# Kernel optimization log

Measured on AMD Instinct MI355X. Metric: run time of the kernel, lower is better.

## Reference

```python
import jax, jax.numpy as jnp
import numpy as np

B, S, HID = 2, 2048, 2048
NH, NKV, HD = 32, 8, 64
EPS = 1e-6
SCALE = HD ** -0.5


def rms_norm(x, w, eps=EPS):
    xf = x.astype(jnp.float32)
    var = jnp.mean(xf * xf, axis=-1, keepdims=True)
    return (w * (xf * jax.lax.rsqrt(var + eps))).astype(x.dtype)


def rotate_half(x):
    x1, x2 = jnp.split(x, 2, axis=-1)
    return jnp.concatenate((-x2, x1), axis=-1)


def setup_inputs() -> dict:
    key = jax.random.key(0)
    ks = jax.random.split(key, 8)
    hidden_states = jax.random.normal(ks[0], (B, S, HID), jnp.float32)
    # realistic RoPE tables
    inv_freq = 1.0 / (500000.0 ** (np.arange(0, HD, 2, dtype=np.float32) / HD))
    pos = np.arange(S, dtype=np.float32)
    freqs = np.outer(pos, inv_freq)                      # [S, HD/2]
    emb = np.concatenate([freqs, freqs], axis=-1)        # [S, HD]
    cos = jnp.broadcast_to(jnp.asarray(np.cos(emb)), (B, S, HD))
    sin = jnp.broadcast_to(jnp.asarray(np.sin(emb)), (B, S, HD))
    std = HID ** -0.5
    Wq = jax.random.normal(ks[1], (NH * HD, HID), jnp.float32) * std
    Wk = jax.random.normal(ks[2], (NKV * HD, HID), jnp.float32) * std
    Wv = jax.random.normal(ks[3], (NKV * HD, HID), jnp.float32) * std
    Wo = jax.random.normal(ks[4], (HID, NH * HD), jnp.float32) * std
    q_norm_w = jnp.ones((HD,), jnp.float32)
    k_norm_w = jnp.ones((HD,), jnp.float32)
    return {"hidden_states": hidden_states, "cos": cos, "sin": sin,
            "Wq": Wq, "Wk": Wk, "Wv": Wv, "Wo": Wo,
            "q_norm_w": q_norm_w, "k_norm_w": k_norm_w}


def reference(hidden_states, cos, sin, Wq, Wk, Wv, Wo, q_norm_w, k_norm_w):
    b, s, _ = hidden_states.shape
    # QKV projections (nn.Linear: x @ W.T)
    q = (hidden_states @ Wq.T).reshape(b, s, NH, HD).transpose(0, 2, 1, 3)   # [B,NH,S,D]
    k = (hidden_states @ Wk.T).reshape(b, s, NKV, HD).transpose(0, 2, 1, 3)  # [B,NKV,S,D]
    v = (hidden_states @ Wv.T).reshape(b, s, NKV, HD).transpose(0, 2, 1, 3)
    # per-head QK RMSNorm (use_head_qk_norm=True)
    q = rms_norm(q, q_norm_w)
    k = rms_norm(k, k_norm_w)
    # RoPE, cos/sin broadcast over heads (unsqueeze dim 1)
    c = cos[:, None, :, :]
    sn = sin[:, None, :, :]
    q = q * c + rotate_half(q) * sn
    k = k * c + rotate_half(k) * sn
    # GQA: expand kv heads to query heads
    groups = NH // NKV
    k = jnp.repeat(k, groups, axis=1)
    v = jnp.repeat(v, groups, axis=1)
    # eager SDPA, causal, softmax in fp32
    scores = jnp.einsum('bhqd,bhkd->bhqk', q, k) * SCALE
    causal = jnp.tril(jnp.ones((s, s), bool))
    scores = jnp.where(causal, scores, jnp.finfo(jnp.float32).min)
    probs = jax.nn.softmax(scores.astype(jnp.float32), axis=-1).astype(q.dtype)
    attn = jnp.einsum('bhqk,bhkd->bhqd', probs, v)       # [B,NH,S,D]
    attn = attn.transpose(0, 2, 1, 3).reshape(b, s, NH * HD)
    return attn @ Wo.T
```

## Files before the change

### kernel.cpp

```cpp
#include <hip/hip_runtime.h>
#include <hip/hip_bf16.h>
#include <stdint.h>

typedef __bf16 bf16;
typedef __bf16 bf16x4 __attribute__((ext_vector_type(4)));
typedef __bf16 bf16x8 __attribute__((ext_vector_type(8)));
typedef float floatx4 __attribute__((ext_vector_type(4)));
typedef float floatx8 __attribute__((ext_vector_type(8)));

#define MFMA16(A, B, C) __builtin_amdgcn_mfma_f32_16x16x32_bf16(A, B, C, 0, 0, 0)

constexpr int Sc = 2048, HIDc = 2048, NHc = 32, NKVc = 8, HDc = 64;
constexpr float kScale = 0.125f;
constexpr float kMax = 9.0f;

__device__ __forceinline__ void async16(const bf16* g, bf16* l) {
  __builtin_amdgcn_global_load_lds(
      (const __attribute__((address_space(1))) void*)g,
      (__attribute__((address_space(3))) void*)l, 16, 0, 0);
}

__global__ __launch_bounds__(256)
void cvt5(const float* __restrict__ s0, bf16* __restrict__ d0, int n0,
          const float* __restrict__ s1, bf16* __restrict__ d1, int n1,
          const float* __restrict__ s2, bf16* __restrict__ d2, int n2,
          const float* __restrict__ s3, bf16* __restrict__ d3, int n3,
          const float* __restrict__ s4, bf16* __restrict__ d4, int n4)
{
  const float* s; bf16* d; int n;
  switch (blockIdx.y) {
    case 0: s = s0; d = d0; n = n0; break;
    case 1: s = s1; d = d1; n = n1; break;
    case 2: s = s2; d = d2; n = n2; break;
    case 3: s = s3; d = d3; n = n3; break;
    default: s = s4; d = d4; n = n4; break;
  }
  const size_t stride = (size_t)gridDim.x * blockDim.x * 8;
  for (size_t i = ((size_t)blockIdx.x * blockDim.x + threadIdx.x) * 8;
       i < (size_t)n; i += stride) {
    floatx8 f = *(const floatx8*)(s + i);
    bf16x8 o;
#pragma unroll
    for (int j = 0; j < 8; ++j) o[j] = (bf16)f[j];
    *(bf16x8*)(d + i) = o;
  }
}

__device__ __forceinline__
void gemm128_core(const bf16* __restrict__ A, const bf16* __restrict__ Bw,
                  int K, int m0, int n0, bf16* __restrict__ lds,
                  floatx4 (&acc)[4][4])
{
  constexpr int IH = 128 * 32;

  const int tid  = threadIdx.x;
  const int lane = tid & 63;
  const int w    = tid >> 6;
  const int r    = lane & 15;
  const int quad = lane >> 4;
  const int wm   = w >> 1;
  const int wn   = w & 1;
  const int NT   = K >> 6;

  const bf16* gA[2]; const bf16* gB[2];
#pragma unroll
  for (int i = 0; i < 2; ++i) {
    const int ch = i * 256 + tid;
    const int lrow = ch >> 3, sl = (ch & 7) ^ (lrow & 7);
    gA[i] = A  + (size_t)(m0 + (sl >> 2) * 64 + lrow) * K + (sl & 3) * 8;
    gB[i] = Bw + (size_t)(n0 + (sl >> 2) * 64 + lrow) * K + (sl & 3) * 8;
  }

  auto stA = [&](int kt, int s, int kk) {
    bf16* dst = lds + (s * 2 + kk) * IH + tid * 8;
#pragma unroll
    for (int i = 0; i < 2; ++i)
      async16(gA[i] + kt * 64 + kk * 32, dst + i * 2048);
  };
  auto stB = [&](int kt, int s, int kk) {
    bf16* dst = lds + 4 * IH + (s * 2 + kk) * IH + tid * 8;
#pragma unroll
    for (int i = 0; i < 2; ++i)
      async16(gB[i] + kt * 64 + kk * 32, dst + i * 2048);
  };

  const int aoff = r * 64 + (((wm << 2) + quad) ^ (r & 7)) * 8;
  const int boff = r * 64 + (((wn << 2) + quad) ^ (r & 7)) * 8;

  bf16x8 a[4], b[4];

#define LDA(S, KK) do { const bf16* _p = lds + ((S) * 2 + (KK)) * IH + aoff; \
  _Pragma("unroll") for (int m2 = 0; m2 < 4; ++m2) a[m2] = *(const bf16x8*)(_p + m2 * 1024); } while (0)
#define LDB(S, KK) do { const bf16* _p = lds + 4 * IH + ((S) * 2 + (KK)) * IH + boff; \
  _Pragma("unroll") for (int n2 = 0; n2 < 4; ++n2) b[n2] = *(const bf16x8*)(_p + n2 * 1024); } while (0)
#define MM() do { __builtin_amdgcn_s_setprio(1); \
  _Pragma("unroll") for (int m2 = 0; m2 < 4; ++m2) \
    _Pragma("unroll") for (int n2 = 0; n2 < 4; ++n2) \
      acc[m2][n2] = MFMA16(a[m2], b[n2], acc[m2][n2]); \
  __builtin_amdgcn_s_setprio(0); } while (0)
#define BAR() asm volatile("s_barrier" ::: "memory")

  stA(0, 0, 0); stB(0, 0, 0); stA(0, 0, 1); stB(0, 0, 1);
  stA(1, 1, 0); stB(1, 1, 0);
  asm volatile("s_waitcnt vmcnt(4)" ::: "memory"); BAR();

  for (int t = 0; t < NT; ++t) {
    const int s = t & 1;
    LDA(s, 0); LDB(s, 0);
    if (t + 1 < NT) { stA(t + 1, s ^ 1, 1); stB(t + 1, s ^ 1, 1); }
    BAR(); MM(); BAR();
    LDA(s, 1); LDB(s, 1);
    if (t + 2 < NT) { stA(t + 2, s, 0); stB(t + 2, s, 0); }
    BAR(); MM();
    if (t + 2 < NT) asm volatile("s_waitcnt vmcnt(4)" ::: "memory");
    else            asm volatile("s_waitcnt vmcnt(0)" ::: "memory");
    BAR();
  }

#undef LDA
#undef LDB
#undef MM
#undef BAR
}

template<bool CF32>
__device__ __forceinline__
void epi_plain(const floatx4 (&acc)[4][4], void* C, int N, int m0, int n0,
               int wm, int wn, int r, int quad)
{
#pragma unroll
  for (int mt = 0; mt < 4; ++mt) {
#pragma unroll
    for (int nt = 0; nt < 4; ++nt) {
      const int row = m0 + wm * 64 + mt * 16 + quad * 4;
      const int col = n0 + wn * 64 + nt * 16 + r;
#pragma unroll
      for (int g = 0; g < 4; ++g) {
        const size_t ci = (size_t)(row + g) * N + col;
        if constexpr (CF32) ((float*)C)[ci] = acc[mt][nt][g];
        else                ((bf16*)C)[ci]  = (bf16)acc[mt][nt][g];
      }
    }
  }
}

__device__ __forceinline__
void epi_k(const floatx4 (&acc)[4][4], bf16* kws, const float* kw,
           const float* cp, const float* sp, int m0, int n0,
           int wm, int wn, int r, int quad)
{
  const int h = (n0 >> 6) + wn;
  const float w0 = kw[r], w1 = kw[16 + r], w2 = kw[32 + r], w3 = kw[48 + r];
#pragma unroll
  for (int mt = 0; mt < 4; ++mt) {
#pragma unroll
    for (int g = 0; g < 4; ++g) {
      const int row = m0 + wm * 64 + mt * 16 + quad * 4 + g;
      const float x0 = acc[mt][0][g], x1 = acc[mt][1][g];
      const float x2 = acc[mt][2][g], x3 = acc[mt][3][g];
      float ss = x0 * x0 + x1 * x1 + x2 * x2 + x3 * x3;
      ss += __shfl_xor(ss, 1); ss += __shfl_xor(ss, 2);
      ss += __shfl_xor(ss, 4); ss += __shfl_xor(ss, 8);
      const float rr = rsqrtf(ss * (1.0f / 64.0f) + 1e-6f);
      const float y0 = x0 * rr * w0, y1 = x1 * rr * w1;
      const float y2 = x2 * rr * w2, y3 = x3 * rr * w3;
      const float* cb = cp + (size_t)row * 64 + r;
      const float* sb = sp + (size_t)row * 64 + r;
      bf16* p = kws + (size_t)row * 512 + h * 64 + r;
      p[0]  = (bf16)(y0 * cb[0]  - y2 * sb[0]);
      p[16] = (bf16)(y1 * cb[16] - y3 * sb[16]);
      p[32] = (bf16)(y2 * cb[32] + y0 * sb[32]);
      p[48] = (bf16)(y3 * cb[48] + y1 * sb[48]);
    }
  }
}

__device__ __forceinline__
void epi_v(const floatx4 (&acc)[4][4], bf16* vt, int m0, int n0,
           int wm, int wn, int r, int quad)
{
  const int kvh = (n0 >> 6) + wn;
  const int b   = m0 >> 11;
  const int sb  = (m0 & 2047) + wm * 64 + quad * 4;
#pragma unroll
  for (int mt = 0; mt < 4; ++mt) {
#pragma unroll
    for (int nt = 0; nt < 4; ++nt) {
      const int d = nt * 16 + r;
      bf16x4 pk;
#pragma unroll
      for (int g = 0; g < 4; ++g) pk[g] = (bf16)acc[mt][nt][g];
      *(bf16x4*)(vt + ((size_t)((b * 8 + kvh) * 64 + d)) * Sc + sb + mt * 16) = pk;
    }
  }
}

__global__ __launch_bounds__(256, 2)
void qkv_gemm8(const bf16* __restrict__ hs,
               const bf16* __restrict__ Wq, const bf16* __restrict__ Wk,
               const bf16* __restrict__ Wv,
               bf16* __restrict__ q_ws, bf16* __restrict__ k_ws,
               bf16* __restrict__ vt_ws,
               const float* __restrict__ kw, const float* __restrict__ cp,
               const float* __restrict__ sp)
{
  __shared__ bf16 lds[8 * 128 * 32];
  const int wg  = blockIdx.x;
  const int swz = (wg & 7) * 96 + (wg >> 3);
  const int mi  = swz / 24, ni = swz % 24;
  const bf16* Bw; int n0;
  if (ni < 16)      { Bw = Wq; n0 = ni * 128; }
  else if (ni < 20) { Bw = Wk; n0 = (ni - 16) * 128; }
  else              { Bw = Wv; n0 = (ni - 20) * 128; }

  floatx4 acc[4][4] = {};
  gemm128_core(hs, Bw, HIDc, mi * 128, n0, lds, acc);

  const int lane = threadIdx.x & 63, w = threadIdx.x >> 6;
  const int r = lane & 15, quad = lane >> 4;
  const int wm = w >> 1, wn = w & 1;
  if (ni < 16)
    epi_plain<false>(acc, q_ws, 2048, mi * 128, n0, wm, wn, r, quad);
  else if (ni < 20)
    epi_k(acc, k_ws, kw, cp, sp, mi * 128, n0, wm, wn, r, quad);
  else
    epi_v(acc, vt_ws, mi * 128, n0, wm, wn, r, quad);
}

__global__ __launch_bounds__(256, 2)
void o_gemm8(const bf16* __restrict__ a_ws, const bf16* __restrict__ Wo,
             float* __restrict__ out)
{
  __shared__ bf16 lds[8 * 128 * 32];
  const int wg  = blockIdx.x;
  const int swz = (wg & 7) * 64 + (wg >> 3);
  const int mi  = swz >> 4, ni = swz & 15;

  floatx4 acc[4][4] = {};
  gemm128_core(a_ws, Wo, NHc * HDc, mi * 128, ni * 128, lds, acc);

  const int lane = threadIdx.x & 63, w = threadIdx.x >> 6;
  const int r = lane & 15, quad = lane >> 4;
  const int wm = w >> 1, wn = w & 1;
  epi_plain<true>(acc, out, HIDc, mi * 128, ni * 128, wm, wn, r, quad);
}

__global__ __launch_bounds__(256, 4)
void attn_fwd(const bf16* __restrict__ q, const bf16* __restrict__ k,
              const bf16* __restrict__ vt, bf16* __restrict__ o,
              const float* __restrict__ qw, const float* __restrict__ cp,
              const float* __restrict__ sp)
{
  __shared__ bf16 Ks[64 * 64];
  __shared__ bf16 Vs[64 * 64];
  __shared__ bf16 Ps[4][16 * 72];

  const int bi  = blockIdx.x;
  const int pa  = bi & 15;
  const int h   = (bi >> 4) & 31;
  const int b   = bi >> 9;
  const int kvh = h >> 2;
  const int tid = threadIdx.x, lane = tid & 63, w = tid >> 6;
  const int r = lane & 15, quad = lane >> 4;
  const int qt0 = 31 - pa, qt1 = pa;

  const floatx8 w0 = *(const floatx8*)(qw + quad * 8);
  const floatx8 w1 = *(const floatx8*)(qw + 32 + quad * 8);
  bf16x8 qf[2][2];
#pragma unroll
  for (int t = 0; t < 2; ++t) {
    const int qt = t == 0 ? qt0 : qt1;
    const int m = b * Sc + qt * 64 + w * 16 + r;
    const bf16* qp = q + (size_t)m * (NHc * HDc) + h * HDc + quad * 8;
    bf16x8 x0 = *(const bf16x8*)qp;
    bf16x8 x1 = *(const bf16x8*)(qp + 32);
    float ss = 0.f;
#pragma unroll
    for (int i = 0; i < 8; ++i)
      ss += (float)x0[i] * (float)x0[i] + (float)x1[i] * (float)x1[i];
    ss += __shfl_xor(ss, 16);
    ss += __shfl_xor(ss, 32);
    const float rq = rsqrtf(ss * (1.0f / 64.0f) + 1e-6f) * kScale;
    const floatx8 c0 = *(const floatx8*)(cp + (size_t)m * 64 + quad * 8);
    const floatx8 c1 = *(const floatx8*)(cp + (size_t)m * 64 + 32 + quad * 8);
    const floatx8 s0 = *(const floatx8*)(sp + (size_t)m * 64 + quad * 8);
    const floatx8 s1 = *(const floatx8*)(sp + (size_t)m * 64 + 32 + quad * 8);
    bf16x8 y0v, y1v;
#pragma unroll
    for (int i = 0; i < 8; ++i) {
      const float y0 = (float)x0[i] * rq * w0[i];
      const float y1 = (float)x1[i] * rq * w1[i];
      y0v[i] = (bf16)(y0 * c0[i] - y1 * s0[i]);
      y1v[i] = (bf16)(y1 * c1[i] + y0 * s1[i]);
    }
    qf[t][0] = y0v; qf[t][1] = y1v;
  }

  floatx4 accO[2][4] = {};
  float lsum[2][4] = {};

  const int kvr = tid >> 3;
  const int cx  = ((tid & 7) * 8) ^ (8 * (kvr & 7));
  const int xk  = 8 * (r & 7);

  const bf16* kp = k + (size_t)b * Sc * (NKVc * HDc) + kvh * HDc;
  const bf16* vp = vt + ((size_t)((b * NKVc + kvh) * 64)) * Sc;

  for (int j = 0; j <= qt0; ++j) {
    __syncthreads();
    {
      const bf16* kj = kp + (size_t)j * 64 * (NKVc * HDc);
      const bf16* vj = vp + j * 64;
      async16(kj + (size_t)kvr * (NKVc * HDc) + cx, Ks + tid * 8);
      async16(kj + (size_t)(kvr + 32) * (NKVc * HDc) + cx, Ks + (tid + 256) * 8);
      async16(vj + (size_t)kvr * Sc + cx, Vs + tid * 8);
      async16(vj + (size_t)(kvr + 32) * Sc + cx, Vs + (tid + 256) * 8);
    }
    __syncthreads();

#pragma unroll
    for (int t = 0; t < 2; ++t) {
      if (t == 1 && j > qt1) continue;
      const int qt = t == 0 ? qt0 : qt1;

      floatx4 sa[4];
#pragma unroll
      for (int nt = 0; nt < 4; ++nt) sa[nt] = floatx4{0.f, 0.f, 0.f, 0.f};
      __builtin_amdgcn_s_setprio(1);
#pragma unroll
      for (int nt = 0; nt < 4; ++nt) {
        const int kv = nt * 16 + r;
        const bf16x8 kb0 = *(const bf16x8*)(&Ks[kv * 64 + ((quad * 8) ^ xk)]);
        const bf16x8 kb1 = *(const bf16x8*)(&Ks[kv * 64 + ((quad * 8 + 32) ^ xk)]);
        sa[nt] = MFMA16(qf[t][0], kb0, sa[nt]);
        sa[nt] = MFMA16(qf[t][1], kb1, sa[nt]);
      }
      __builtin_amdgcn_s_setprio(0);

      if (j != qt) {
#pragma unroll
        for (int g = 0; g < 4; ++g)
#pragma unroll
          for (int nt = 0; nt < 4; ++nt) {
            const float p = __expf(sa[nt][g] - kMax);
            lsum[t][g] += p;
            Ps[w][(quad * 4 + g) * 72 + nt * 16 + r] = (bf16)p;
          }
      } else {
        const int maskbase = w * 16 + quad * 4;
#pragma unroll
        for (int g = 0; g < 4; ++g)
#pragma unroll
          for (int nt = 0; nt < 4; ++nt) {
            const float p = (nt * 16 + r <= maskbase + g)
                                ? __expf(sa[nt][g] - kMax) : 0.f;
            lsum[t][g] += p;
            Ps[w][(quad * 4 + g) * 72 + nt * 16 + r] = (bf16)p;
          }
      }

      const bf16x8 pa0 = *(const bf16x8*)(&Ps[w][r * 72 + quad * 8]);
      const bf16x8 pa1 = *(const bf16x8*)(&Ps[w][r * 72 + 32 + quad * 8]);
      __builtin_amdgcn_s_setprio(1);
#pragma unroll
      for (int dt = 0; dt < 4; ++dt) {
        const int d = dt * 16 + r;
        const bf16x8 vb0 = *(const bf16x8*)(&Vs[d * 64 + ((quad * 8) ^ xk)]);
        const bf16x8 vb1 = *(const bf16x8*)(&Vs[d * 64 + ((quad * 8 + 32) ^ xk)]);
        accO[t][dt] = MFMA16(pa0, vb0, accO[t][dt]);
        accO[t][dt] = MFMA16(pa1, vb1, accO[t][dt]);
      }
      __builtin_amdgcn_s_setprio(0);
    }
  }

#pragma unroll
  for (int t = 0; t < 2; ++t) {
    const int qt = t == 0 ? qt0 : qt1;
#pragma unroll
    for (int reg = 0; reg < 4; ++reg) {
      float l = lsum[t][reg];
#pragma unroll
      for (int off = 1; off < 16; off <<= 1) l += __shfl_xor(l, off);
      const float inv = 1.0f / l;
      const size_t row = (size_t)(b * Sc + qt * 64 + w * 16 + quad * 4 + reg);
#pragma unroll
      for (int dt = 0; dt < 4; ++dt)
        o[row * (NHc * HDc) + h * HDc + dt * 16 + r] = (bf16)(accO[t][dt][reg] * inv);
    }
  }
}

extern "C" void kernel_launch(void* const* d_in, const int* in_sizes, int n_in,
                              void* d_out, int out_size, void* d_ws, size_t ws_size,
                              hipStream_t stream)
{
  const float* hs = (const float*)d_in[0];
  const float* cp = (const float*)d_in[1];
  const float* sp = (const float*)d_in[2];
  const float* Wq = (const float*)d_in[3];
  const float* Wk = (const float*)d_in[4];
  const float* Wv = (const float*)d_in[5];
  const float* Wo = (const float*)d_in[6];
  const float* qw = (const float*)d_in[7];
  const float* kw = (const float*)d_in[8];
  float* out = (float*)d_out;

  char* ws = (char*)d_ws;
  bf16* q_ws  = (bf16*)ws;
  bf16* k_ws  = (bf16*)(ws + (16u << 20));
  bf16* vt_ws = (bf16*)(ws + (24u << 20));
  bf16* hs_b  = (bf16*)(ws + (28u << 20));
  bf16* Wq_b  = (bf16*)(ws + (44u << 20));
  bf16* Wk_b  = (bf16*)(ws + (52u << 20));
  bf16* Wv_b  = (bf16*)(ws + (54u << 20));
  bf16* Wo_b  = (bf16*)(ws + (56u << 20));
  bf16* a_ws  = q_ws;

  dim3 blk(256);
  cvt5<<<dim3(256, 5), blk, 0, stream>>>(
      hs, hs_b, 4096 * 2048, Wq, Wq_b, 2048 * 2048, Wk, Wk_b, 512 * 2048,
      Wv, Wv_b, 512 * 2048, Wo, Wo_b, 2048 * 2048);
  qkv_gemm8<<<dim3(768), blk, 0, stream>>>(hs_b, Wq_b, Wk_b, Wv_b,
                                           q_ws, k_ws, vt_ws, kw, cp, sp);
  attn_fwd<<<dim3(1024), blk, 0, stream>>>(q_ws, k_ws, vt_ws, a_ws, qw, cp, sp);
  o_gemm8<<<dim3(512), blk, 0, stream>>>(a_ws, Wo_b, out);
}
```

Before: 299.0 us.

## Split paired causal q-tiles into one tile per block, longest first

The attention kernel used to give each block two complementary query tiles (qt and 31-qt) that shared each K/V tile load. It now gives each block a single query tile, launches 2048 blocks ordered so the longest causal rows are scheduled first, and raises the occupancy hint from 4 to 6 blocks per CU. Register use and per-block imbalance both drop, and more waves can be resident. In exchange, each K/V tile is loaded from global memory twice as often because the pairing no longer shares it.

```diff
diff --git a/kernel.cpp b/kernel.cpp
--- a/kernel.cpp
+++ b/kernel.cpp
@@ -245,7 +245,7 @@
   epi_plain<true>(acc, out, HIDc, mi * 128, ni * 128, wm, wn, r, quad);
 }
 
-__global__ __launch_bounds__(256, 4)
+__global__ __launch_bounds__(256, 6)
 void attn_fwd(const bf16* __restrict__ q, const bf16* __restrict__ k,
               const bf16* __restrict__ vt, bf16* __restrict__ o,
               const float* __restrict__ qw, const float* __restrict__ cp,
@@ -256,20 +256,18 @@
   __shared__ bf16 Ps[4][16 * 72];
 
   const int bi  = blockIdx.x;
-  const int pa  = bi & 15;
-  const int h   = (bi >> 4) & 31;
-  const int b   = bi >> 9;
+  const int qt  = 31 - (bi >> 6);
+  const int hb  = bi & 63;
+  const int h   = hb & 31;
+  const int b   = hb >> 5;
   const int kvh = h >> 2;
   const int tid = threadIdx.x, lane = tid & 63, w = tid >> 6;
   const int r = lane & 15, quad = lane >> 4;
-  const int qt0 = 31 - pa, qt1 = pa;
 
   const floatx8 w0 = *(const floatx8*)(qw + quad * 8);
   const floatx8 w1 = *(const floatx8*)(qw + 32 + quad * 8);
-  bf16x8 qf[2][2];
-#pragma unroll
-  for (int t = 0; t < 2; ++t) {
-    const int qt = t == 0 ? qt0 : qt1;
+  bf16x8 qf0, qf1;
+  {
     const int m = b * Sc + qt * 64 + w * 16 + r;
     const bf16* qp = q + (size_t)m * (NHc * HDc) + h * HDc + quad * 8;
     bf16x8 x0 = *(const bf16x8*)qp;
@@ -285,19 +283,17 @@
     const floatx8 c1 = *(const floatx8*)(cp + (size_t)m * 64 + 32 + quad * 8);
     const floatx8 s0 = *(const floatx8*)(sp + (size_t)m * 64 + quad * 8);
     const floatx8 s1 = *(const floatx8*)(sp + (size_t)m * 64 + 32 + quad * 8);
-    bf16x8 y0v, y1v;
 #pragma unroll
     for (int i = 0; i < 8; ++i) {
       const float y0 = (float)x0[i] * rq * w0[i];
       const float y1 = (float)x1[i] * rq * w1[i];
-      y0v[i] = (bf16)(y0 * c0[i] - y1 * s0[i]);
-      y1v[i] = (bf16)(y1 * c1[i] + y0 * s1[i]);
-    }
-    qf[t][0] = y0v; qf[t][1] = y1v;
-  }
-
-  floatx4 accO[2][4] = {};
-  float lsum[2][4] = {};
+      qf0[i] = (bf16)(y0 * c0[i] - y1 * s0[i]);
+      qf1[i] = (bf16)(y1 * c1[i] + y0 * s1[i]);
+    }
+  }
+
+  floatx4 accO[4] = {};
+  float lsum[4] = {};
 
   const int kvr = tid >> 3;
   const int cx  = ((tid & 7) * 8) ^ (8 * (kvr & 7));
@@ -306,7 +302,7 @@
   const bf16* kp = k + (size_t)b * Sc * (NKVc * HDc) + kvh * HDc;
   const bf16* vp = vt + ((size_t)((b * NKVc + kvh) * 64)) * Sc;
 
-  for (int j = 0; j <= qt0; ++j) {
+  for (int j = 0; j <= qt; ++j) {
     __syncthreads();
     {
       const bf16* kj = kp + (size_t)j * 64 * (NKVc * HDc);
@@ -318,76 +314,66 @@
     }
     __syncthreads();
 
-#pragma unroll
-    for (int t = 0; t < 2; ++t) {
-      if (t == 1 && j > qt1) continue;
-      const int qt = t == 0 ? qt0 : qt1;
-
-      floatx4 sa[4];
-#pragma unroll
-      for (int nt = 0; nt < 4; ++nt) sa[nt] = floatx4{0.f, 0.f, 0.f, 0.f};
-      __builtin_amdgcn_s_setprio(1);
-#pragma unroll
-      for (int nt = 0; nt < 4; ++nt) {
-        const int kv = nt * 16 + r;
-        const bf16x8 kb0 = *(const bf16x8*)(&Ks[kv * 64 + ((quad * 8) ^ xk)]);
-        const bf16x8 kb1 = *(const bf16x8*)(&Ks[kv * 64 + ((quad * 8 + 32) ^ xk)]);
-        sa[nt] = MFMA16(qf[t][0], kb0, sa[nt]);
-        sa[nt] = MFMA16(qf[t][1], kb1, sa[nt]);
-      }
-      __builtin_amdgcn_s_setprio(0);
-
-      if (j != qt) {
-#pragma unroll
-        for (int g = 0; g < 4; ++g)
-#pragma unroll
-          for (int nt = 0; nt < 4; ++nt) {
-            const float p = __expf(sa[nt][g] - kMax);
-            lsum[t][g] += p;
-            Ps[w][(quad * 4 + g) * 72 + nt * 16 + r] = (bf16)p;
-          }
-      } else {
-        const int maskbase = w * 16 + quad * 4;
-#pragma unroll
-        for (int g = 0; g < 4; ++g)
-#pragma unroll
-          for (int nt = 0; nt < 4; ++nt) {
-            const float p = (nt * 16 + r <= maskbase + g)
-                                ? __expf(sa[nt][g] - kMax) : 0.f;
-            lsum[t][g] += p;
-            Ps[w][(quad * 4 + g) * 72 + nt * 16 + r] = (bf16)p;
-          }
-      }
-
-      const bf16x8 pa0 = *(const bf16x8*)(&Ps[w][r * 72 + quad * 8]);
-      const bf16x8 pa1 = *(const bf16x8*)(&Ps[w][r * 72 + 32 + quad * 8]);
-      __builtin_amdgcn_s_setprio(1);
-#pragma unroll
-      for (int dt = 0; dt < 4; ++dt) {
-        const int d = dt * 16 + r;
-        const bf16x8 vb0 = *(const bf16x8*)(&Vs[d * 64 + ((quad * 8) ^ xk)]);
-        const bf16x8 vb1 = *(const bf16x8*)(&Vs[d * 64 + ((quad * 8 + 32) ^ xk)]);
-        accO[t][dt] = MFMA16(pa0, vb0, accO[t][dt]);
-        accO[t][dt] = MFMA16(pa1, vb1, accO[t][dt]);
-      }
-      __builtin_amdgcn_s_setprio(0);
-    }
-  }
-
-#pragma unroll
-  for (int t = 0; t < 2; ++t) {
-    const int qt = t == 0 ? qt0 : qt1;
-#pragma unroll
-    for (int reg = 0; reg < 4; ++reg) {
-      float l = lsum[t][reg];
-#pragma unroll
-      for (int off = 1; off < 16; off <<= 1) l += __shfl_xor(l, off);
-      const float inv = 1.0f / l;
-      const size_t row = (size_t)(b * Sc + qt * 64 + w * 16 + quad * 4 + reg);
-#pragma unroll
-      for (int dt = 0; dt < 4; ++dt)
-        o[row * (NHc * HDc) + h * HDc + dt * 16 + r] = (bf16)(accO[t][dt][reg] * inv);
-    }
+    floatx4 sa[4];
+#pragma unroll
+    for (int nt = 0; nt < 4; ++nt) sa[nt] = floatx4{0.f, 0.f, 0.f, 0.f};
+    __builtin_amdgcn_s_setprio(1);
+#pragma unroll
+    for (int nt = 0; nt < 4; ++nt) {
+      const int kv = nt * 16 + r;
+      const bf16x8 kb0 = *(const bf16x8*)(&Ks[kv * 64 + ((quad * 8) ^ xk)]);
+      const bf16x8 kb1 = *(const bf16x8*)(&Ks[kv * 64 + ((quad * 8 + 32) ^ xk)]);
+      sa[nt] = MFMA16(qf0, kb0, sa[nt]);
+      sa[nt] = MFMA16(qf1, kb1, sa[nt]);
+    }
+    __builtin_amdgcn_s_setprio(0);
+
+    if (j != qt) {
+#pragma unroll
+      for (int g = 0; g < 4; ++g)
+#pragma unroll
+        for (int nt = 0; nt < 4; ++nt) {
+          const float p = __expf(sa[nt][g] - kMax);
+          lsum[g] += p;
+          Ps[w][(quad * 4 + g) * 72 + nt * 16 + r] = (bf16)p;
+        }
+    } else {
+      const int maskbase = w * 16 + quad * 4;
+#pragma unroll
+      for (int g = 0; g < 4; ++g)
+#pragma unroll
+        for (int nt = 0; nt < 4; ++nt) {
+          const float p = (nt * 16 + r <= maskbase + g)
+                              ? __expf(sa[nt][g] - kMax) : 0.f;
+          lsum[g] += p;
+          Ps[w][(quad * 4 + g) * 72 + nt * 16 + r] = (bf16)p;
+        }
+    }
+
+    const bf16x8 pa0 = *(const bf16x8*)(&Ps[w][r * 72 + quad * 8]);
+    const bf16x8 pa1 = *(const bf16x8*)(&Ps[w][r * 72 + 32 + quad * 8]);
+    __builtin_amdgcn_s_setprio(1);
+#pragma unroll
+    for (int dt = 0; dt < 4; ++dt) {
+      const int d = dt * 16 + r;
+      const bf16x8 vb0 = *(const bf16x8*)(&Vs[d * 64 + ((quad * 8) ^ xk)]);
+      const bf16x8 vb1 = *(const bf16x8*)(&Vs[d * 64 + ((quad * 8 + 32) ^ xk)]);
+      accO[dt] = MFMA16(pa0, vb0, accO[dt]);
+      accO[dt] = MFMA16(pa1, vb1, accO[dt]);
+    }
+    __builtin_amdgcn_s_setprio(0);
+  }
+
+#pragma unroll
+  for (int reg = 0; reg < 4; ++reg) {
+    float l = lsum[reg];
+#pragma unroll
+    for (int off = 1; off < 16; off <<= 1) l += __shfl_xor(l, off);
+    const float inv = 1.0f / l;
+    const size_t row = (size_t)(b * Sc + qt * 64 + w * 16 + quad * 4 + reg);
+#pragma unroll
+    for (int dt = 0; dt < 4; ++dt)
+      o[row * (NHc * HDc) + h * HDc + dt * 16 + r] = (bf16)(accO[dt][reg] * inv);
   }
 }
 
@@ -423,6 +409,6 @@
       Wv, Wv_b, 512 * 2048, Wo, Wo_b, 2048 * 2048);
   qkv_gemm8<<<dim3(768), blk, 0, stream>>>(hs_b, Wq_b, Wk_b, Wv_b,
                                            q_ws, k_ws, vt_ws, kw, cp, sp);
-  attn_fwd<<<dim3(1024), blk, 0, stream>>>(q_ws, k_ws, vt_ws, a_ws, qw, cp, sp);
+  attn_fwd<<<dim3(2048), blk, 0, stream>>>(q_ws, k_ws, vt_ws, a_ws, qw, cp, sp);
   o_gemm8<<<dim3(512), blk, 0, stream>>>(a_ws, Wo_b, out);
 }
```

Result: no change. 296.4 us (-0.9%).
